# Kernel tuning notes

Measured on AMD Instinct MI355X. Metric: run time of the kernel, lower is better.

Reference implementation:

```python
import jax, jax.numpy as jnp
import numpy as np

ALPHA = 0.3


def _maxsim_scores(q, d):
    # q: [B, N, D], d: [C, S, D] -> scores [B, C]
    # MaxSim: per (query b, doc c), sum over query tokens of max over doc tokens.
    sim = jnp.einsum('bnd,csd->bcns', q, d)  # [B, C, N, S]
    return sim.max(axis=3).sum(axis=2)       # [B, C]


def setup_inputs() -> dict:
    key = jax.random.key(0)
    k1, k2, k3, k4 = jax.random.split(key, 4)
    B, N, S, D = 64, 32, 1024, 128
    return {
        'query_embeddings': jax.random.normal(k1, (B, N, D), dtype=jnp.float32),
        'doc_embeddings': jax.random.normal(k2, (B, S, D), dtype=jnp.float32),
        'teacher_query_outputs': jax.random.normal(k3, (B, N, D), dtype=jnp.float32),
        'teacher_doc_outputs': jax.random.normal(k4, (B, S, D), dtype=jnp.float32),
    }


def reference(query_embeddings, doc_embeddings, teacher_query_outputs, teacher_doc_outputs):
    scores = _maxsim_scores(query_embeddings, doc_embeddings)  # [B, B]
    B = scores.shape[0]
    pos_scores = jnp.diag(scores)                               # [B]
    eye = jnp.eye(B, dtype=bool)
    s_masked = jnp.where(eye, -jnp.inf, scores)
    neg_scores = s_masked.max(axis=1)                           # hardest negative per query
    contrastive_loss = jax.nn.softplus(neg_scores - pos_scores).mean()

    teacher_scores = _maxsim_scores(teacher_query_outputs, teacher_doc_outputs)
    # Torch MSELoss on fp16-cast inputs: compute in fp16, then promote.
    diff16 = scores.astype(jnp.float16) - teacher_scores.astype(jnp.float16)
    mse_loss = jnp.mean(diff16 * diff16).astype(jnp.float32)

    return contrastive_loss + ALPHA * mse_loss
```

## Files before the change

### kernel.cpp

```cpp
#include <hip/hip_runtime.h>
#include <hip/hip_bf16.h>

typedef __attribute__((ext_vector_type(8))) short short8;
typedef __attribute__((ext_vector_type(4))) float floatx4;

#define B_SZ   64
#define N_TOK  32
#define S_TOK  1024
#define D_DIM  128
#define ALPHA  0.3f

#define STRIP_S     32
#define STRIP_EL    (STRIP_S * D_DIM)
#define STRIP_BYTES (STRIP_EL * 2)
#define NSTRIP      (S_TOK / STRIP_S)
#define NBUF        6
#define C_EL        (S_TOK * D_DIM)

#define DBLK (B_SZ * S_TOK * D_DIM / 8 / 256)
#define QBLK (B_SZ * N_TOK * D_DIM / 8 / 256)

#define WAITV_(N) asm volatile("s_waitcnt vmcnt(" #N ")" ::: "memory")
#define WAITV(N)  WAITV_(N)

__device__ __forceinline__ short f2bf(float f) {
    __hip_bfloat16 h = __float2bfloat16(f);
    return __builtin_bit_cast(short, h);
}

__device__ __forceinline__ short8 cvt8(const float* __restrict__ p) {
    floatx4 f0 = *reinterpret_cast<const floatx4*>(p);
    floatx4 f1 = *reinterpret_cast<const floatx4*>(p + 4);
    short8 r;
    r[0] = f2bf(f0[0]); r[1] = f2bf(f0[1]); r[2] = f2bf(f0[2]); r[3] = f2bf(f0[3]);
    r[4] = f2bf(f1[0]); r[5] = f2bf(f1[1]); r[6] = f2bf(f1[2]); r[7] = f2bf(f1[3]);
    return r;
}

__global__ __launch_bounds__(256) void cvt_all_kernel(
    const float* __restrict__ q,  const float* __restrict__ d,
    const float* __restrict__ tq, const float* __restrict__ td,
    __hip_bfloat16* __restrict__ qb,  __hip_bfloat16* __restrict__ db,
    __hip_bfloat16* __restrict__ tqb, __hip_bfloat16* __restrict__ tdb) {
    const int which = blockIdx.y;
    if (blockIdx.x >= DBLK) {
        const float* src = which ? tq : q;
        __hip_bfloat16* dst = which ? tqb : qb;
        int idx = (blockIdx.x - DBLK) * 256 + threadIdx.x;
        *reinterpret_cast<short8*>(dst + (size_t)idx * 8) = cvt8(src + (size_t)idx * 8);
    } else {
        const float* src = which ? td : d;
        __hip_bfloat16* dst = which ? tdb : db;
        int idx = blockIdx.x * 256 + threadIdx.x;
        int kc = idx & 15;
        int s  = (idx >> 4) & (S_TOK - 1);
        int c  = idx >> 14;
        int st = s >> 5, nt = (s >> 4) & 1, lr = s & 15;
        int ks = kc >> 2, lg = kc & 3;
        size_t dpos = (size_t)c * C_EL + (size_t)st * STRIP_EL
                    + (size_t)(ks * 2 + nt) * 512 + (size_t)(lg * 16 + lr) * 8;
        *reinterpret_cast<short8*>(dst + dpos) = cvt8(src + (size_t)idx * 8);
    }
}

__device__ __forceinline__ void gload_lds16(const void* g, void* l) {
    __builtin_amdgcn_global_load_lds(
        (const __attribute__((address_space(1))) unsigned int*)g,
        (__attribute__((address_space(3))) unsigned int*)l, 16, 0, 0);
}

__global__ __launch_bounds__(256, 2) void maxsim_scores_kernel(
    const __hip_bfloat16* __restrict__ qb,  const __hip_bfloat16* __restrict__ db,
    const __hip_bfloat16* __restrict__ tqb, const __hip_bfloat16* __restrict__ tdb,
    float* __restrict__ scores_ws ) {

    const int c     = blockIdx.x;
    const int bg    = blockIdx.y;
    const int which = blockIdx.z;
    const __hip_bfloat16* Q = which ? tqb : qb;
    const __hip_bfloat16* D = which ? tdb : db;
    float* out = scores_ws + which * (B_SZ * B_SZ);

    const int tid = threadIdx.x;
    const int w   = tid >> 6;
    const int l   = tid & 63;
    const int lg  = l >> 4;
    const int lr  = l & 15;

    const int b0 = bg * 16 + w * 4;

    __shared__ __align__(16) char smem[NBUF * STRIP_BYTES];

    short8 afrag[8][4];
#pragma unroll
    for (int mt = 0; mt < 8; ++mt)
#pragma unroll
        for (int ks = 0; ks < 4; ++ks)
            afrag[mt][ks] = *reinterpret_cast<const short8*>(
                Q + ((size_t)(b0 + (mt >> 1)) * N_TOK + (mt & 1) * 16 + lr) * D_DIM
                  + ks * 32 + lg * 8);
#pragma unroll
    for (int mt = 0; mt < 8; ++mt)
#pragma unroll
        for (int ks = 0; ks < 4; ++ks)
            asm volatile("" : "+v"(afrag[mt][ks]));

    float runmax[8][4];
#pragma unroll
    for (int mt = 0; mt < 8; ++mt)
#pragma unroll
        for (int j = 0; j < 4; ++j) runmax[mt][j] = -INFINITY;

    const char* gstrip = (const char*)(D + (size_t)c * C_EL);
    const unsigned y0 = tid * 16;
    const unsigned y1 = 4096 + tid * 16;

#pragma unroll
    for (int p = 0; p < 3; ++p) {
        gload_lds16(gstrip + p * STRIP_BYTES + y0, smem + p * STRIP_BYTES + y0);
        gload_lds16(gstrip + p * STRIP_BYTES + y1, smem + p * STRIP_BYTES + y1);
    }

    auto compute = [&](const char* bufc) {
#pragma unroll
        for (int nt = 0; nt < 2; ++nt) {
            short8 bf[4];
#pragma unroll
            for (int ks = 0; ks < 4; ++ks)
                bf[ks] = *reinterpret_cast<const short8*>(
                    bufc + (ks * 2 + nt) * 1024 + l * 16);

            floatx4 acc[8];
#pragma unroll
            for (int mt = 0; mt < 8; ++mt) acc[mt] = floatx4{0.f, 0.f, 0.f, 0.f};

#pragma unroll
            for (int ks = 0; ks < 4; ++ks)
#pragma unroll
                for (int mt = 0; mt < 8; ++mt)
                    acc[mt] = __builtin_amdgcn_mfma_f32_16x16x32_bf16(
                        afrag[mt][ks], bf[ks], acc[mt], 0, 0, 0);

#pragma unroll
            for (int mt = 0; mt < 8; ++mt)
#pragma unroll
                for (int j = 0; j < 4; ++j)
                    runmax[mt][j] = fmaxf(runmax[mt][j], acc[mt][j]);
        }
    };

    for (int st = 0; st < NSTRIP - 3; ++st) {
        const int tb = (st + 3) % NBUF;
        const char* gs = gstrip + (size_t)(st + 3) * STRIP_BYTES;
        gload_lds16(gs + y0, smem + tb * STRIP_BYTES + y0);
        gload_lds16(gs + y1, smem + tb * STRIP_BYTES + y1);
        WAITV(6);
        __builtin_amdgcn_s_barrier();
        compute(smem + (st % NBUF) * STRIP_BYTES);
    }
    WAITV(4);
    __builtin_amdgcn_s_barrier();
    compute(smem + ((NSTRIP - 3) % NBUF) * STRIP_BYTES);
    WAITV(2);
    __builtin_amdgcn_s_barrier();
    compute(smem + ((NSTRIP - 2) % NBUF) * STRIP_BYTES);
    WAITV(0);
    __builtin_amdgcn_s_barrier();
    compute(smem + ((NSTRIP - 1) % NBUF) * STRIP_BYTES);

#pragma unroll
    for (int mt = 0; mt < 8; ++mt)
#pragma unroll
        for (int j = 0; j < 4; ++j) {
            float v = runmax[mt][j];
            v = fmaxf(v, __shfl_xor(v, 1));
            v = fmaxf(v, __shfl_xor(v, 2));
            v = fmaxf(v, __shfl_xor(v, 4));
            v = fmaxf(v, __shfl_xor(v, 8));
            runmax[mt][j] = v;
        }

#pragma unroll
    for (int p = 0; p < 4; ++p) {
        float s = 0.f;
#pragma unroll
        for (int j = 0; j < 4; ++j) s += runmax[2 * p][j] + runmax[2 * p + 1][j];
        s += __shfl_xor(s, 16);
        s += __shfl_xor(s, 32);
        if (l == 0) out[(b0 + p) * B_SZ + c] = s;
    }
}

__global__ void loss_kernel(const float* __restrict__ scores_ws, float* __restrict__ out) {
    const float* sc = scores_ws;
    const float* tc = scores_ws + B_SZ * B_SZ;
    const int b = threadIdx.x;

    float pos = sc[b * B_SZ + b];
    float neg = -INFINITY;
    float msesum = 0.f;
#pragma unroll 8
    for (int cc = 0; cc < B_SZ; ++cc) {
        float s = sc[b * B_SZ + cc];
        float t = tc[b * B_SZ + cc];
        if (cc != b) neg = fmaxf(neg, s);
        _Float16 d16 = (_Float16)s - (_Float16)t;
        _Float16 sq  = d16 * d16;
        msesum += (float)sq;
    }
    float x = neg - pos;
    float sp = (x > 0.f) ? (x + log1pf(expf(-x))) : log1pf(expf(x));

#pragma unroll
    for (int m = 1; m < 64; m <<= 1) {
        sp     += __shfl_xor(sp, m);
        msesum += __shfl_xor(msesum, m);
    }
    if (b == 0) {
        float mse = msesum / 4096.f;
        mse = (float)(_Float16)mse;
        out[0] = sp / 64.f + ALPHA * mse;
    }
}

extern "C" void kernel_launch(void* const* d_in, const int* in_sizes, int n_in,
                              void* d_out, int out_size, void* d_ws, size_t ws_size,
                              hipStream_t stream) {
    const float* q  = (const float*)d_in[0];
    const float* d  = (const float*)d_in[1];
    const float* tq = (const float*)d_in[2];
    const float* td = (const float*)d_in[3];
    float* out = (float*)d_out;

    const size_t QN = (size_t)B_SZ * N_TOK * D_DIM;
    const size_t DN = (size_t)B_SZ * S_TOK * D_DIM;

    float* scores_ws = (float*)d_ws;
    __hip_bfloat16* qb  = (__hip_bfloat16*)((char*)d_ws + 32768);
    __hip_bfloat16* tqb = qb + QN;
    __hip_bfloat16* db  = tqb + QN;
    __hip_bfloat16* tdb = db + DN;

    cvt_all_kernel<<<dim3(DBLK + QBLK, 2), 256, 0, stream>>>(
        q, d, tq, td, qb, db, tqb, tdb);

    dim3 grid(B_SZ, B_SZ / 16, 2);
    maxsim_scores_kernel<<<grid, 256, 0, stream>>>(qb, db, tqb, tdb, scores_ws);
    loss_kernel<<<1, 64, 0, stream>>>(scores_ws, out);
}
```

Before: 74.45 us.

## Restructure strip pipeline with ping-pong barriers, setprio, and fewer LDS buffers

Rewrites the main strip loop so each strip is split into two half-tiles. Each half loads its B fragments from LDS, then waits at a barrier before a high-priority MFMA burst (s_setprio), with sched_barrier fencing. This mimics the ping-pong scheduling pattern in which waves alternate between memory and MFMA phases. The LDS ring shrinks from 6 to 4 buffers and the global prefetch is issued mid-iteration, with wait counts adjusted per iteration. It adds several extra barriers per strip, which risks serialization, in exchange for better MFMA/memory interleaving and lower LDS use that could allow higher occupancy.

After: 76.18 us. 1.02x slower.

```diff
diff --git a/kernel.cpp b/kernel.cpp
--- a/kernel.cpp
+++ b/kernel.cpp
@@ -14,7 +14,7 @@
 #define STRIP_EL    (STRIP_S * D_DIM)
 #define STRIP_BYTES (STRIP_EL * 2)
 #define NSTRIP      (S_TOK / STRIP_S)
-#define NBUF        6
+#define NBUF        4
 #define C_EL        (S_TOK * D_DIM)
 
 #define DBLK (B_SZ * S_TOK * D_DIM / 8 / 256)
@@ -111,62 +111,90 @@
 #pragma unroll
         for (int j = 0; j < 4; ++j) runmax[mt][j] = -INFINITY;
 
+    const floatx4 fzero = {0.f, 0.f, 0.f, 0.f};
+
     const char* gstrip = (const char*)(D + (size_t)c * C_EL);
     const unsigned y0 = tid * 16;
     const unsigned y1 = 4096 + tid * 16;
 
 #pragma unroll
     for (int p = 0; p < 3; ++p) {
-        gload_lds16(gstrip + p * STRIP_BYTES + y0, smem + p * STRIP_BYTES + y0);
-        gload_lds16(gstrip + p * STRIP_BYTES + y1, smem + p * STRIP_BYTES + y1);
-    }
-
-    auto compute = [&](const char* bufc) {
-#pragma unroll
-        for (int nt = 0; nt < 2; ++nt) {
-            short8 bf[4];
-#pragma unroll
-            for (int ks = 0; ks < 4; ++ks)
-                bf[ks] = *reinterpret_cast<const short8*>(
-                    bufc + (ks * 2 + nt) * 1024 + l * 16);
-
-            floatx4 acc[8];
-#pragma unroll
-            for (int mt = 0; mt < 8; ++mt) acc[mt] = floatx4{0.f, 0.f, 0.f, 0.f};
-
-#pragma unroll
-            for (int ks = 0; ks < 4; ++ks)
-#pragma unroll
-                for (int mt = 0; mt < 8; ++mt)
-                    acc[mt] = __builtin_amdgcn_mfma_f32_16x16x32_bf16(
-                        afrag[mt][ks], bf[ks], acc[mt], 0, 0, 0);
-
-#pragma unroll
-            for (int mt = 0; mt < 8; ++mt)
-#pragma unroll
-                for (int j = 0; j < 4; ++j)
-                    runmax[mt][j] = fmaxf(runmax[mt][j], acc[mt][j]);
-        }
-    };
-
-    for (int st = 0; st < NSTRIP - 3; ++st) {
-        const int tb = (st + 3) % NBUF;
-        const char* gs = gstrip + (size_t)(st + 3) * STRIP_BYTES;
-        gload_lds16(gs + y0, smem + tb * STRIP_BYTES + y0);
-        gload_lds16(gs + y1, smem + tb * STRIP_BYTES + y1);
-        WAITV(6);
-        __builtin_amdgcn_s_barrier();
-        compute(smem + (st % NBUF) * STRIP_BYTES);
+        gload_lds16(gstrip + (size_t)p * STRIP_BYTES + y0, smem + p * STRIP_BYTES + y0);
+        gload_lds16(gstrip + (size_t)p * STRIP_BYTES + y1, smem + p * STRIP_BYTES + y1);
     }
     WAITV(4);
     __builtin_amdgcn_s_barrier();
-    compute(smem + ((NSTRIP - 3) % NBUF) * STRIP_BYTES);
-    WAITV(2);
-    __builtin_amdgcn_s_barrier();
-    compute(smem + ((NSTRIP - 2) % NBUF) * STRIP_BYTES);
-    WAITV(0);
-    __builtin_amdgcn_s_barrier();
-    compute(smem + ((NSTRIP - 1) % NBUF) * STRIP_BYTES);
+
+    for (int st = 0; st < NSTRIP; ++st) {
+        const char* bufc = smem + (size_t)(st & (NBUF - 1)) * STRIP_BYTES;
+
+        short8 bf0[4];
+#pragma unroll
+        for (int ks = 0; ks < 4; ++ks)
+            bf0[ks] = *reinterpret_cast<const short8*>(bufc + (ks * 2) * 1024 + l * 16);
+
+        if (st < NSTRIP - 3) {
+            const char* gs = gstrip + (size_t)(st + 3) * STRIP_BYTES;
+            char* bufn = smem + (size_t)((st + 3) & (NBUF - 1)) * STRIP_BYTES;
+            gload_lds16(gs + y0, bufn + y0);
+            gload_lds16(gs + y1, bufn + y1);
+        }
+
+        __builtin_amdgcn_s_barrier();
+        asm volatile("s_waitcnt lgkmcnt(0)" ::: "memory");
+        __builtin_amdgcn_sched_barrier(0);
+        __builtin_amdgcn_s_setprio(1);
+        floatx4 acc[8];
+#pragma unroll
+        for (int mt = 0; mt < 8; ++mt)
+            acc[mt] = __builtin_amdgcn_mfma_f32_16x16x32_bf16(
+                afrag[mt][0], bf0[0], fzero, 0, 0, 0);
+#pragma unroll
+        for (int ks = 1; ks < 4; ++ks)
+#pragma unroll
+            for (int mt = 0; mt < 8; ++mt)
+                acc[mt] = __builtin_amdgcn_mfma_f32_16x16x32_bf16(
+                    afrag[mt][ks], bf0[ks], acc[mt], 0, 0, 0);
+        __builtin_amdgcn_s_setprio(0);
+#pragma unroll
+        for (int mt = 0; mt < 8; ++mt)
+#pragma unroll
+            for (int j = 0; j < 4; ++j)
+                runmax[mt][j] = fmaxf(runmax[mt][j], acc[mt][j]);
+        __builtin_amdgcn_s_barrier();
+
+        short8 bf1[4];
+#pragma unroll
+        for (int ks = 0; ks < 4; ++ks)
+            bf1[ks] = *reinterpret_cast<const short8*>(bufc + (ks * 2 + 1) * 1024 + l * 16);
+
+        __builtin_amdgcn_s_barrier();
+        asm volatile("s_waitcnt lgkmcnt(0)" ::: "memory");
+        __builtin_amdgcn_sched_barrier(0);
+        __builtin_amdgcn_s_setprio(1);
+        floatx4 acc1[8];
+#pragma unroll
+        for (int mt = 0; mt < 8; ++mt)
+            acc1[mt] = __builtin_amdgcn_mfma_f32_16x16x32_bf16(
+                afrag[mt][0], bf1[0], fzero, 0, 0, 0);
+#pragma unroll
+        for (int ks = 1; ks < 4; ++ks)
+#pragma unroll
+            for (int mt = 0; mt < 8; ++mt)
+                acc1[mt] = __builtin_amdgcn_mfma_f32_16x16x32_bf16(
+                    afrag[mt][ks], bf1[ks], acc1[mt], 0, 0, 0);
+        __builtin_amdgcn_s_setprio(0);
+#pragma unroll
+        for (int mt = 0; mt < 8; ++mt)
+#pragma unroll
+            for (int j = 0; j < 4; ++j)
+                runmax[mt][j] = fmaxf(runmax[mt][j], acc1[mt][j]);
+
+        if (st < NSTRIP - 3)       WAITV(4);
+        else if (st == NSTRIP - 3) WAITV(2);
+        else if (st == NSTRIP - 2) WAITV(0);
+        __builtin_amdgcn_s_barrier();
+    }
 
 #pragma unroll
     for (int mt = 0; mt < 8; ++mt)
```
